# Kernel tuning notes

Hardware: AMD Instinct MI355X
Metric: run time of the kernel (lower is better)

## Reference

```python
import jax, jax.numpy as jnp
import numpy as np

STEP_SIZE = 0.01  # init kwarg step_size

def _quad_grad(A, b, x):
    # grad of per-node quadratic: 2*A_n @ x_n + b_n ; shapes [N,D,D],[N,D],[N,D]
    return 2.0 * jnp.einsum('nij,nj->ni', A, x) + b

def setup_inputs() -> dict:
    key = jax.random.key(0)
    kA, kb, kx, ke = jax.random.split(key, 4)
    N, D, E = 20000, 64, 320000
    A = jax.random.normal(kA, (N, D, D), dtype=jnp.float32)
    b = jax.random.normal(kb, (N, D), dtype=jnp.float32)
    x = jax.random.normal(kx, (N, D), dtype=jnp.float32)
    edge_index = jax.random.randint(ke, (2, E), 0, N, dtype=jnp.int64)
    return {"A": A, "b": b, "x": x, "edge_index": edge_index, "num_layers": 10}

def reference(A, b, x, edge_index, num_layers):
    N, D = x.shape
    src, dst = edge_index[0], edge_index[1]
    # push-sum column-stochastic mixing weights: 1/out_degree incl. self-loop
    deg = jnp.ones((N,), x.dtype).at[src].add(1.0)
    inv_deg = (1.0 / deg)[:, None]  # [N,1]

    def mix(z):  # z: [N,F]
        msg = z[src] * inv_deg[src]  # gather + weight
        agg = jax.ops.segment_sum(msg, dst, num_segments=N)
        return agg + z * inv_deg  # self-loop term

    y = _quad_grad(A, b, x)
    u = x
    v = jnp.ones((N, 1), x.dtype)
    x0 = x
    x1 = x0
    for _ in range(num_layers):
        u = mix(u - STEP_SIZE * y)          # conv on u
        v = mix(v)                           # conv on v (push-sum weight)
        x1 = u * (1.0 / v)                   # inv_v * u
        g1 = _quad_grad(A, b, x1)
        g0 = _quad_grad(A, b, x0)
        y = mix(y) + g1 - g0                 # conv on y + gradient tracking
        x0 = x1
    comm_cost = jnp.asarray(3 * num_layers * src.shape[0], dtype=jnp.int64)
    return x1, comm_cost
```

## Files before the change

### kernel.cpp

```cpp
#include <hip/hip_runtime.h>
#include <hip/hip_bf16.h>
#include <hip/hip_fp16.h>

#define STEP 0.01f
#define D 64
#define NUM_LAYERS 10

union H4 { uint2 u; __half h[4]; };
union H8 { uint4 u; __half2 h2[4]; __half h[8]; };

typedef float f32x2 __attribute__((ext_vector_type(2)));


__global__ void k_setup(float* __restrict__ degf, int* __restrict__ degd, int N) {
    int n = blockIdx.x * blockDim.x + threadIdx.x;
    if (n < N) { degf[n] = 1.0f; degd[n] = 0; }
}

__global__ void k_deg2(const int* __restrict__ ei, float* __restrict__ degf,
                       int* __restrict__ degd, int E) {
    int e = blockIdx.x * blockDim.x + threadIdx.x;
    if (e < E) {
        unsafeAtomicAdd(&degf[ei[e]], 1.0f);
        atomicAdd(&degd[ei[E + e]], 1);
    }
}

__global__ __launch_bounds__(1024) void k_scan(
        const int* __restrict__ degd, const float* __restrict__ degf,
        int* __restrict__ row_ptr, int* __restrict__ cursor,
        float* __restrict__ invdeg, int N, int E) {
    __shared__ int part[1024];
    int tid = threadIdx.x;
    int chunk = (N + 1023) / 1024;
    int lo = tid * chunk, hi = min(lo + chunk, N);
    int s = 0;
    for (int i = lo; i < hi; ++i) s += degd[i];
    part[tid] = s;
    __syncthreads();
    for (int off = 1; off < 1024; off <<= 1) {
        int v = (tid >= off) ? part[tid - off] : 0;
        __syncthreads();
        part[tid] += v;
        __syncthreads();
    }
    int base = (tid == 0) ? 0 : part[tid - 1];
    for (int i = lo; i < hi; ++i) {
        row_ptr[i] = base;
        cursor[i] = base;
        base += degd[i];
        invdeg[i] = 1.0f / degf[i];
    }
    if (tid == 1023) row_ptr[N] = E;
}

__global__ void k_scatter(const int* __restrict__ ei, int* __restrict__ cursor,
                          int* __restrict__ col, int E) {
    int e = blockIdx.x * blockDim.x + threadIdx.x;
    if (e < E) {
        int pos = atomicAdd(&cursor[ei[E + e]], 1);
        col[pos] = ei[e];
    }
}


__global__ __launch_bounds__(256) void k_init(
        const float* __restrict__ A, const float* __restrict__ b,
        const float* __restrict__ x, const float* __restrict__ invdeg,
        unsigned char* __restrict__ Ah8, __half2* __restrict__ msg,
        float* __restrict__ vw, float* __restrict__ x0, int N) {
    __shared__ __align__(16) float sx[D];
    __shared__ float syv[D];
    int n = blockIdx.x, t = threadIdx.x;
    int lane = t & 63, w = t >> 6, colgrp = lane & 15;
    if (t < D) sx[t] = x[(size_t)n * D + t];
    __syncthreads();
    const float* An = A + (size_t)n * D * D;
    unsigned char* A8n = Ah8 + (size_t)n * D * D;
    float4 xr = ((const float4*)sx)[colgrp];
    int rbase = w * 16 + (lane >> 4);
#pragma unroll
    for (int g = 0; g < 4; ++g) {
        int row = rbase + g * 4;
        float4 a = ((const float4*)(An + (size_t)row * D))[colgrp];
        int d8 = __builtin_amdgcn_cvt_pk_fp8_f32(a.x, a.y, 0, false);
        d8 = __builtin_amdgcn_cvt_pk_fp8_f32(a.z, a.w, d8, true);
        ((unsigned int*)(A8n + (size_t)row * D))[colgrp] = (unsigned int)d8;
        float p = a.x * xr.x + a.y * xr.y + a.z * xr.z + a.w * xr.w;
        p += __shfl_xor(p, 1);
        p += __shfl_xor(p, 2);
        p += __shfl_xor(p, 4);
        p += __shfl_xor(p, 8);
        if (colgrp == 0) syv[row] = 2.0f * p + b[(size_t)n * D + row];
    }
    __syncthreads();
    if (t < D) {
        float wd = invdeg[n];
        float xv = sx[t];
        float yv = syv[t];
        msg[(size_t)n * D + t] = __floats2half2_rn((xv - STEP * yv) * wd, yv * wd);
        x0[(size_t)n * D + t] = xv;
        if (t == 0) vw[n] = wd;
    }
}


__global__ __launch_bounds__(256) void k_layer(
        const unsigned char* __restrict__ Ah8,
        const int* __restrict__ row_ptr, const int* __restrict__ col,
        const __half2* __restrict__ msg, const float* __restrict__ vw,
        const float* __restrict__ invdeg,
        __half2* __restrict__ msgn, float* __restrict__ vwn,
        float* __restrict__ x0, float* __restrict__ xout,
        int last_idx, float comm, int N) {
    __shared__ float su[4][D];
    __shared__ float sy[4][D];
    __shared__ float sv[4];
    __shared__ __align__(16) float sdx[D];
    __shared__ float sun[D];
    __shared__ float sytot[D];
    __shared__ float syn[D];
    __shared__ float svn;

    int n = blockIdx.x, t = threadIdx.x;
    int lane = t & 63, w = t >> 6;
    int j = lane >> 4, q4 = lane & 15;

    int rs = row_ptr[n], re = row_ptr[n + 1];
    float4 au = {0.f, 0.f, 0.f, 0.f}, ay = {0.f, 0.f, 0.f, 0.f};
    float av = 0.0f;
    for (int base = rs + w * 4; base < re; base += 16) {
        int e = base + j;
        if (e < re) {
            int s = col[e];
            H8 m;
            m.u = ((const uint4*)(msg + (size_t)s * D))[q4];
            float2 f0 = __half22float2(m.h2[0]);
            float2 f1 = __half22float2(m.h2[1]);
            float2 f2 = __half22float2(m.h2[2]);
            float2 f3 = __half22float2(m.h2[3]);
            au.x += f0.x; ay.x += f0.y;
            au.y += f1.x; ay.y += f1.y;
            au.z += f2.x; ay.z += f2.y;
            au.w += f3.x; ay.w += f3.y;
            if (q4 == 0) av += vw[s];
        }
    }
    au.x += __shfl_xor(au.x, 16); au.y += __shfl_xor(au.y, 16);
    au.z += __shfl_xor(au.z, 16); au.w += __shfl_xor(au.w, 16);
    au.x += __shfl_xor(au.x, 32); au.y += __shfl_xor(au.y, 32);
    au.z += __shfl_xor(au.z, 32); au.w += __shfl_xor(au.w, 32);
    ay.x += __shfl_xor(ay.x, 16); ay.y += __shfl_xor(ay.y, 16);
    ay.z += __shfl_xor(ay.z, 16); ay.w += __shfl_xor(ay.w, 16);
    ay.x += __shfl_xor(ay.x, 32); ay.y += __shfl_xor(ay.y, 32);
    ay.z += __shfl_xor(ay.z, 32); ay.w += __shfl_xor(ay.w, 32);
    av += __shfl_xor(av, 16);
    av += __shfl_xor(av, 32);
    if (j == 0) {
        ((float4*)su[w])[q4] = au;
        ((float4*)sy[w])[q4] = ay;
        if (q4 == 0) sv[w] = av;
    }
    __syncthreads();

    if (w == 0) {
        size_t off = (size_t)n * D + lane;
        float2 self = __half22float2(msg[off]);
        float ut = su[0][lane] + su[1][lane] + su[2][lane] + su[3][lane] + self.x;
        float yt = sy[0][lane] + sy[1][lane] + sy[2][lane] + sy[3][lane] + self.y;
        float vt = sv[0] + sv[1] + sv[2] + sv[3] + vw[n];
        float x1 = ut / vt;
        sdx[lane] = x1 - x0[off];
        x0[off] = x1;
        if (xout) xout[off] = x1;
        sun[lane] = ut;
        sytot[lane] = yt;
        if (lane == 0) svn = vt;
    }
    __syncthreads();

    {
        const uint2* Ahp = (const uint2*)(Ah8 + (size_t)n * D * D);
        int cb = (t & 7) * 8;
        int r0 = t >> 3;
        uint2 a0 = Ahp[t];
        uint2 a1 = Ahp[256 + t];
        float p0 = 0.0f, p1 = 0.0f;
        f32x2 q;
        q = __builtin_amdgcn_cvt_pk_f32_fp8((int)a0.x, false);
        p0 += q.x * sdx[cb + 0] + q.y * sdx[cb + 1];
        q = __builtin_amdgcn_cvt_pk_f32_fp8((int)a0.x, true);
        p0 += q.x * sdx[cb + 2] + q.y * sdx[cb + 3];
        q = __builtin_amdgcn_cvt_pk_f32_fp8((int)a0.y, false);
        p0 += q.x * sdx[cb + 4] + q.y * sdx[cb + 5];
        q = __builtin_amdgcn_cvt_pk_f32_fp8((int)a0.y, true);
        p0 += q.x * sdx[cb + 6] + q.y * sdx[cb + 7];
        q = __builtin_amdgcn_cvt_pk_f32_fp8((int)a1.x, false);
        p1 += q.x * sdx[cb + 0] + q.y * sdx[cb + 1];
        q = __builtin_amdgcn_cvt_pk_f32_fp8((int)a1.x, true);
        p1 += q.x * sdx[cb + 2] + q.y * sdx[cb + 3];
        q = __builtin_amdgcn_cvt_pk_f32_fp8((int)a1.y, false);
        p1 += q.x * sdx[cb + 4] + q.y * sdx[cb + 5];
        q = __builtin_amdgcn_cvt_pk_f32_fp8((int)a1.y, true);
        p1 += q.x * sdx[cb + 6] + q.y * sdx[cb + 7];
        p0 += __shfl_xor(p0, 1); p1 += __shfl_xor(p1, 1);
        p0 += __shfl_xor(p0, 2); p1 += __shfl_xor(p1, 2);
        p0 += __shfl_xor(p0, 4); p1 += __shfl_xor(p1, 4);
        if ((lane & 7) == 0) {
            syn[r0]      = sytot[r0]      + 2.0f * p0;
            syn[32 + r0] = sytot[32 + r0] + 2.0f * p1;
        }
    }
    __syncthreads();

    if (t < D) {
        float wd = invdeg[n];
        float ynf = syn[t];
        msgn[(size_t)n * D + t] = __floats2half2_rn((sun[t] - STEP * ynf) * wd, ynf * wd);
        if (t == 0) vwn[n] = svn * wd;
    }
    if (xout && n == 0 && t == 0) xout[last_idx] = comm;
}


extern "C" void kernel_launch(void* const* d_in, const int* in_sizes, int n_in,
                              void* d_out, int out_size, void* d_ws, size_t ws_size,
                              hipStream_t stream) {
    const float* A  = (const float*)d_in[0];
    const float* b  = (const float*)d_in[1];
    const float* x  = (const float*)d_in[2];
    const int*   ei = (const int*)d_in[3];

    const int N = in_sizes[1] / D;
    const int E = in_sizes[3] / 2;
    const size_t ND = (size_t)N * D;

    char* ws = (char*)d_ws;
    unsigned char* Ah8 = (unsigned char*)ws;
    __half2* msg0 = (__half2*)(ws + ND * D);
    __half2* msg1 = msg0 + ND;
    float* x0   = (float*)(msg1 + ND);
    float* vw0  = x0 + ND;
    float* vw1  = vw0 + N;
    float* invdeg = vw1 + N;
    float* degf = invdeg + N;
    int* degd    = (int*)(degf + N);
    int* row_ptr = degd + N;
    int* cursor  = row_ptr + N + 4;
    int* col     = cursor + N;

    k_setup<<<(N + 255) / 256, 256, 0, stream>>>(degf, degd, N);
    k_deg2<<<(E + 255) / 256, 256, 0, stream>>>(ei, degf, degd, E);
    k_scan<<<1, 1024, 0, stream>>>(degd, degf, row_ptr, cursor, invdeg, N, E);
    k_scatter<<<(E + 255) / 256, 256, 0, stream>>>(ei, cursor, col, E);
    k_init<<<N, 256, 0, stream>>>(A, b, x, invdeg, Ah8, msg0, vw0, x0, N);

    float comm = (float)(3 * NUM_LAYERS * E);
    __half2 *mc = msg0, *mn = msg1;
    float *vc = vw0, *vn = vw1;
    for (int l = 0; l < NUM_LAYERS; ++l) {
        float* xout = (l == NUM_LAYERS - 1) ? (float*)d_out : nullptr;
        k_layer<<<N, 256, 0, stream>>>(Ah8, row_ptr, col, mc, vc, invdeg,
                                       mn, vn, x0, xout, out_size - 1, comm, N);
        __half2* tm = mc; mc = mn; mn = tm;
        float* tv = vc; vc = vn; vn = tv;
    }
}
```

Before: 928.6 us.

## Replace shared-memory staging in layer kernel with redundant per-wave compute and shuffles

Every wave now redundantly computes the aggregated u, y, v and dx for all 64 features, where previously only wave 0 did. The A-matrix matvec then broadcasts dx through warp shuffles instead of shared memory, and each wave handles 16 rows with 16-byte loads. This removes two __syncthreads barriers and several shared arrays. A, x0, the self message, vw and invdeg are loaded before the neighbor gather so their latency overlaps with it, at the cost of extra shuffles and redundant arithmetic.

```diff
diff --git a/kernel.cpp b/kernel.cpp
--- a/kernel.cpp
+++ b/kernel.cpp
@@ -116,15 +116,18 @@
     __shared__ float su[4][D];
     __shared__ float sy[4][D];
     __shared__ float sv[4];
-    __shared__ __align__(16) float sdx[D];
-    __shared__ float sun[D];
-    __shared__ float sytot[D];
-    __shared__ float syn[D];
-    __shared__ float svn;
 
     int n = blockIdx.x, t = threadIdx.x;
     int lane = t & 63, w = t >> 6;
     int j = lane >> 4, q4 = lane & 15;
+
+    size_t off = (size_t)n * D + lane;
+    const uint4* Ap = (const uint4*)(Ah8 + (size_t)n * D * D);
+    uint4 a4 = Ap[(((w << 4) + (lane >> 2)) << 2) + (lane & 3)];
+    float2 self = __half22float2(msg[off]);
+    float x0v = x0[off];
+    float vwself = vw[n];
+    float invd = invdeg[n];
 
     int rs = row_ptr[n], re = row_ptr[n + 1];
     float4 au = {0.f, 0.f, 0.f, 0.f}, ay = {0.f, 0.f, 0.f, 0.f};
@@ -163,63 +166,62 @@
     }
     __syncthreads();
 
+    float ut = su[0][lane] + su[1][lane] + su[2][lane] + su[3][lane] + self.x;
+    float yt = sy[0][lane] + sy[1][lane] + sy[2][lane] + sy[3][lane] + self.y;
+    float vt = sv[0] + sv[1] + sv[2] + sv[3] + vwself;
+    float x1 = ut / vt;
+    float dx = x1 - x0v;
     if (w == 0) {
-        size_t off = (size_t)n * D + lane;
-        float2 self = __half22float2(msg[off]);
-        float ut = su[0][lane] + su[1][lane] + su[2][lane] + su[3][lane] + self.x;
-        float yt = sy[0][lane] + sy[1][lane] + sy[2][lane] + sy[3][lane] + self.y;
-        float vt = sv[0] + sv[1] + sv[2] + sv[3] + vw[n];
-        float x1 = ut / vt;
-        sdx[lane] = x1 - x0[off];
         x0[off] = x1;
-        if (xout) xout[off] = x1;
-        sun[lane] = ut;
-        sytot[lane] = yt;
-        if (lane == 0) svn = vt;
-    }
-    __syncthreads();
-
+        if (xout) {
+            xout[off] = x1;
+            if (n == 0 && lane == 0) xout[last_idx] = comm;
+        }
+        if (lane == 0) vwn[n] = vt * invd;
+    }
+
+    int c0 = (lane & 3) << 4;
+    float p = 0.0f;
     {
-        const uint2* Ahp = (const uint2*)(Ah8 + (size_t)n * D * D);
-        int cb = (t & 7) * 8;
-        int r0 = t >> 3;
-        uint2 a0 = Ahp[t];
-        uint2 a1 = Ahp[256 + t];
-        float p0 = 0.0f, p1 = 0.0f;
         f32x2 q;
-        q = __builtin_amdgcn_cvt_pk_f32_fp8((int)a0.x, false);
-        p0 += q.x * sdx[cb + 0] + q.y * sdx[cb + 1];
-        q = __builtin_amdgcn_cvt_pk_f32_fp8((int)a0.x, true);
-        p0 += q.x * sdx[cb + 2] + q.y * sdx[cb + 3];
-        q = __builtin_amdgcn_cvt_pk_f32_fp8((int)a0.y, false);
-        p0 += q.x * sdx[cb + 4] + q.y * sdx[cb + 5];
-        q = __builtin_amdgcn_cvt_pk_f32_fp8((int)a0.y, true);
-        p0 += q.x * sdx[cb + 6] + q.y * sdx[cb + 7];
-        q = __builtin_amdgcn_cvt_pk_f32_fp8((int)a1.x, false);
-        p1 += q.x * sdx[cb + 0] + q.y * sdx[cb + 1];
-        q = __builtin_amdgcn_cvt_pk_f32_fp8((int)a1.x, true);
-        p1 += q.x * sdx[cb + 2] + q.y * sdx[cb + 3];
-        q = __builtin_amdgcn_cvt_pk_f32_fp8((int)a1.y, false);
-        p1 += q.x * sdx[cb + 4] + q.y * sdx[cb + 5];
-        q = __builtin_amdgcn_cvt_pk_f32_fp8((int)a1.y, true);
-        p1 += q.x * sdx[cb + 6] + q.y * sdx[cb + 7];
-        p0 += __shfl_xor(p0, 1); p1 += __shfl_xor(p1, 1);
-        p0 += __shfl_xor(p0, 2); p1 += __shfl_xor(p1, 2);
-        p0 += __shfl_xor(p0, 4); p1 += __shfl_xor(p1, 4);
-        if ((lane & 7) == 0) {
-            syn[r0]      = sytot[r0]      + 2.0f * p0;
-            syn[32 + r0] = sytot[32 + r0] + 2.0f * p1;
-        }
-    }
-    __syncthreads();
-
-    if (t < D) {
-        float wd = invdeg[n];
-        float ynf = syn[t];
-        msgn[(size_t)n * D + t] = __floats2half2_rn((sun[t] - STEP * ynf) * wd, ynf * wd);
-        if (t == 0) vwn[n] = svn * wd;
-    }
-    if (xout && n == 0 && t == 0) xout[last_idx] = comm;
+        float d0, d1;
+        q = __builtin_amdgcn_cvt_pk_f32_fp8((int)a4.x, false);
+        d0 = __shfl(dx, c0 + 0);  d1 = __shfl(dx, c0 + 1);
+        p += q.x * d0 + q.y * d1;
+        q = __builtin_amdgcn_cvt_pk_f32_fp8((int)a4.x, true);
+        d0 = __shfl(dx, c0 + 2);  d1 = __shfl(dx, c0 + 3);
+        p += q.x * d0 + q.y * d1;
+        q = __builtin_amdgcn_cvt_pk_f32_fp8((int)a4.y, false);
+        d0 = __shfl(dx, c0 + 4);  d1 = __shfl(dx, c0 + 5);
+        p += q.x * d0 + q.y * d1;
+        q = __builtin_amdgcn_cvt_pk_f32_fp8((int)a4.y, true);
+        d0 = __shfl(dx, c0 + 6);  d1 = __shfl(dx, c0 + 7);
+        p += q.x * d0 + q.y * d1;
+        q = __builtin_amdgcn_cvt_pk_f32_fp8((int)a4.z, false);
+        d0 = __shfl(dx, c0 + 8);  d1 = __shfl(dx, c0 + 9);
+        p += q.x * d0 + q.y * d1;
+        q = __builtin_amdgcn_cvt_pk_f32_fp8((int)a4.z, true);
+        d0 = __shfl(dx, c0 + 10); d1 = __shfl(dx, c0 + 11);
+        p += q.x * d0 + q.y * d1;
+        q = __builtin_amdgcn_cvt_pk_f32_fp8((int)a4.w, false);
+        d0 = __shfl(dx, c0 + 12); d1 = __shfl(dx, c0 + 13);
+        p += q.x * d0 + q.y * d1;
+        q = __builtin_amdgcn_cvt_pk_f32_fp8((int)a4.w, true);
+        d0 = __shfl(dx, c0 + 14); d1 = __shfl(dx, c0 + 15);
+        p += q.x * d0 + q.y * d1;
+    }
+    p += __shfl_xor(p, 1);
+    p += __shfl_xor(p, 2);
+
+    float prow = __shfl(p, (lane << 2) & 63);
+    int si = ((w << 4) + lane) & 63;
+    float und = __shfl(ut, si);
+    float ytd = __shfl(yt, si);
+    if (lane < 16) {
+        float yn = ytd + 2.0f * prow;
+        msgn[(size_t)n * D + (w << 4) + lane] =
+            __floats2half2_rn((und - STEP * yn) * invd, yn * invd);
+    }
 }
 
 
```

Result: slower. 979.9 us (+5.5%).
